# Kernel optimization log

Hardware: AMD Instinct MI355X
Metric: run time of the kernel (lower is better)

Reference implementation:

```python
import jax, jax.numpy as jnp
import numpy as np

N_HEADS = 16
ROPE_DIMS = 64


def _rope_tables(T, rd):
    # freqs: 1 / 10000^(arange(0, rd, 2)/rd), shape [rd//2]
    freqs = 1.0 / (10000.0 ** (np.arange(0, rd, 2, dtype=np.float32) / np.float32(rd)))
    ang = np.outer(np.arange(T, dtype=np.float32), freqs)  # [T, rd//2]
    return jnp.asarray(np.cos(ang)), jnp.asarray(np.sin(ang))


def _apply_rope(x, cos, sin, rd):
    # x: [B, H, T, D]; rotate-half style on first rd dims
    x_rope, x_pass = x[..., :rd], x[..., rd:]
    x1, x2 = x_rope[..., : rd // 2], x_rope[..., rd // 2 :]
    c = cos[None, None]  # [1,1,T,rd//2]
    s = sin[None, None]
    x_rot = jnp.concatenate([x1 * c - x2 * s, x2 * c + x1 * s], axis=-1)
    return jnp.concatenate([x_rot, x_pass], axis=-1)


def setup_inputs() -> dict:
    key = jax.random.key(0)
    k1, k2, k3 = jax.random.split(key, 3)
    B, T, C = 32, 512, 2048
    x = jax.random.normal(k1, (B, T, C), dtype=jnp.float32)
    w_qkv = jax.random.normal(k2, (3 * C, C), dtype=jnp.float32) * 0.02
    w_out = jax.random.normal(k3, (C, C), dtype=jnp.float32) * 0.02
    return {"x": x, "w_qkv": w_qkv, "w_out": w_out}


def reference(x, w_qkv, w_out):
    B, T, C = x.shape
    H = N_HEADS
    D = C // H
    # fused QKV projection: F.linear(x, w) = x @ w.T
    qkv = jnp.einsum('btc,fc->btf', x, w_qkv).reshape(B, T, 3, H, D)
    q = jnp.transpose(qkv[:, :, 0], (0, 2, 1, 3))  # [B,H,T,D]
    k = jnp.transpose(qkv[:, :, 1], (0, 2, 1, 3))
    v = jnp.transpose(qkv[:, :, 2], (0, 2, 1, 3))
    cos, sin = _rope_tables(T, ROPE_DIMS)
    q = _apply_rope(q, cos, sin, ROPE_DIMS)
    k = _apply_rope(k, cos, sin, ROPE_DIMS)
    # causal SDPA
    scale = 1.0 / jnp.sqrt(jnp.asarray(D, dtype=x.dtype))
    scores = jnp.einsum('bhqd,bhkd->bhqk', q, k) * scale
    causal = jnp.tril(jnp.ones((T, T), dtype=bool))
    scores = jnp.where(causal[None, None], scores, jnp.finfo(scores.dtype).min)
    attn = jax.nn.softmax(scores, axis=-1)
    y = jnp.einsum('bhqk,bhkd->bhqd', attn, v)
    y = jnp.transpose(y, (0, 2, 1, 3)).reshape(B, T, C)
    return jnp.einsum('btc,fc->btf', y, w_out)
```

## Files before the change

kernel.cpp:

```cpp
#include <hip/hip_runtime.h>


typedef __bf16 bf16x8 __attribute__((ext_vector_type(8)));
typedef float floatx4 __attribute__((ext_vector_type(4)));

__device__ __forceinline__ unsigned short f2bf(float f) {
  union { float f; unsigned u; } v; v.f = f;
  unsigned r = v.u + 0x7FFFu + ((v.u >> 16) & 1u);
  return (unsigned short)(r >> 16);
}
__device__ __forceinline__ float bf2f(unsigned short h) {
  union { unsigned u; float f; } v; v.u = ((unsigned)h) << 16; return v.f;
}

__device__ __forceinline__ void load_lds16(const void* g, void* l) {
  __builtin_amdgcn_global_load_lds((__attribute__((address_space(1))) void*)g,
                                   (__attribute__((address_space(3))) void*)l,
                                   16, 0, 0);
}

__global__ void rope_tables(float* __restrict__ cost, float* __restrict__ sint) {
  int i = blockIdx.x * 256 + threadIdx.x;
  if (i >= 512 * 32) return;
  int t = i >> 5, f = i & 31;
  float e = -(float)(2 * f) / 64.0f;
  float freq = powf(10000.0f, e);
  float ang = (float)t * freq;
  cost[i] = cosf(ang);
  sint[i] = sinf(ang);
}

__global__ void cast_bf16(const float* __restrict__ in,
                          unsigned short* __restrict__ out, int n8) {
  int i = blockIdx.x * 256 + threadIdx.x;
  if (i >= n8) return;
  float4 a = ((const float4*)in)[2 * i];
  float4 b = ((const float4*)in)[2 * i + 1];
  union { uint4 v; unsigned short u[8]; } o;
  o.u[0] = f2bf(a.x); o.u[1] = f2bf(a.y); o.u[2] = f2bf(a.z); o.u[3] = f2bf(a.w);
  o.u[4] = f2bf(b.x); o.u[5] = f2bf(b.y); o.u[6] = f2bf(b.z); o.u[7] = f2bf(b.w);
  ((uint4*)out)[i] = o.v;
}

template <int OUT_BF16>
__global__ __launch_bounds__(256) void gemm_bt(
    const unsigned short* __restrict__ A, const unsigned short* __restrict__ Bt,
    void* __restrict__ Cout, int M, int N, int K) {
  __shared__ __align__(16) unsigned short As[128 * 64];
  __shared__ __align__(16) unsigned short Bs[128 * 64];
  const int tid = threadIdx.x;
  const int bn = blockIdx.x, bm = blockIdx.y;
  const int w = tid >> 6, l = tid & 63;
  const int quad = l >> 4, cl = l & 15;
  const int m_base = (w & 1) * 64, n_base = (w >> 1) * 64;
  floatx4 acc[4][4] = {};

  const int srow = tid >> 3;
  const int sc = (tid & 7) ^ (srow & 7);
  const unsigned short* Ag = A + (size_t)(bm * 128 + srow) * K + sc * 8;
  const unsigned short* Bg = Bt + (size_t)(bn * 128 + srow) * K + sc * 8;
  unsigned short* asd = As + tid * 8;
  unsigned short* bsd = Bs + tid * 8;

  for (int kt = 0; kt < K; kt += 64) {
    __syncthreads();
#pragma unroll
    for (int i = 0; i < 4; ++i) {
      load_lds16(Ag + (size_t)i * 32 * K + kt, asd + i * 32 * 64);
      load_lds16(Bg + (size_t)i * 32 * K + kt, bsd + i * 32 * 64);
    }
    __syncthreads();
#pragma unroll
    for (int k0 = 0; k0 < 64; k0 += 32) {
      const int xs = (((k0 >> 3) + quad) ^ (cl & 7)) << 3;
      bf16x8 a[4], b[4];
#pragma unroll
      for (int mt = 0; mt < 4; ++mt)
        a[mt] = *(const bf16x8*)(As + (m_base + mt * 16 + cl) * 64 + xs);
#pragma unroll
      for (int nt = 0; nt < 4; ++nt)
        b[nt] = *(const bf16x8*)(Bs + (n_base + nt * 16 + cl) * 64 + xs);
#pragma unroll
      for (int mt = 0; mt < 4; ++mt)
#pragma unroll
        for (int nt = 0; nt < 4; ++nt)
          acc[mt][nt] = __builtin_amdgcn_mfma_f32_16x16x32_bf16(
              a[mt], b[nt], acc[mt][nt], 0, 0, 0);
    }
  }
#pragma unroll
  for (int mt = 0; mt < 4; ++mt)
#pragma unroll
    for (int nt = 0; nt < 4; ++nt)
#pragma unroll
      for (int r = 0; r < 4; ++r) {
        int gm = bm * 128 + m_base + mt * 16 + quad * 4 + r;
        int gn = bn * 128 + n_base + nt * 16 + cl;
        float v = acc[mt][nt][r];
        if (OUT_BF16)
          ((unsigned short*)Cout)[(size_t)gm * N + gn] = f2bf(v);
        else
          ((float*)Cout)[(size_t)gm * N + gn] = v;
      }
}

__global__ __launch_bounds__(256) void attn_kernel(
    const unsigned short* __restrict__ qkv, const float* __restrict__ cost,
    const float* __restrict__ sint, unsigned short* __restrict__ y) {
  __shared__ __align__(16) unsigned short Qs[64][136];
  __shared__ __align__(16) unsigned short Ks[64][136];
  __shared__ __align__(16) unsigned short VTs[128][64];
  __shared__ __align__(16) unsigned short Ps[4][16][72];

  const int bh = blockIdx.x, qt = blockIdx.y;
  const int b = bh >> 4, h = bh & 15;
  const int tid = threadIdx.x, w = tid >> 6, l = tid & 63;
  const int quad = l >> 4, cl = l & 15;
  const float scale = 0.08838834764831845f * 1.4426950408889634f;

  {
    const int r = tid >> 2, j = tid & 3;
    const int tg = qt * 64 + r;
    const unsigned short* qrow = qkv + (size_t)(b * 512 + tg) * 6144 + h * 128;
    union { uint4 v; unsigned short u[8]; } c1, c2, p1, p2, o1, o2, o3, o4;
    c1.v = *(const uint4*)(qrow + j * 8);
    c2.v = *(const uint4*)(qrow + j * 8 + 32);
    p1.v = *(const uint4*)(qrow + 64 + j * 16);
    p2.v = *(const uint4*)(qrow + 64 + j * 16 + 8);
#pragma unroll
    for (int jj = 0; jj < 8; ++jj) {
      int d = j * 8 + jj;
      float c = cost[tg * 32 + d], s = sint[tg * 32 + d];
      float x1 = bf2f(c1.u[jj]), x2 = bf2f(c2.u[jj]);
      o1.u[jj] = f2bf((x1 * c - x2 * s) * scale);
      o2.u[jj] = f2bf((x2 * c + x1 * s) * scale);
      o3.u[jj] = f2bf(bf2f(p1.u[jj]) * scale);
      o4.u[jj] = f2bf(bf2f(p2.u[jj]) * scale);
    }
    *(uint4*)&Qs[r][j * 8]          = o1.v;
    *(uint4*)&Qs[r][j * 8 + 32]     = o2.v;
    *(uint4*)&Qs[r][64 + j * 16]     = o3.v;
    *(uint4*)&Qs[r][64 + j * 16 + 8] = o4.v;
  }

  floatx4 o[8] = {};
  float m_i[4] = {-__builtin_inff(), -__builtin_inff(), -__builtin_inff(),
                  -__builtin_inff()};
  float l_i[4] = {0.f, 0.f, 0.f, 0.f};

  for (int ktile = 0; ktile <= qt; ++ktile) {
    __syncthreads();
    {
      const int r = tid >> 2, j = tid & 3;
      const int tg = ktile * 64 + r;
      const unsigned short* krow =
          qkv + (size_t)(b * 512 + tg) * 6144 + 2048 + h * 128;
      union { uint4 v; unsigned short u[8]; } c1, c2, p1, p2, o1, o2;
      c1.v = *(const uint4*)(krow + j * 8);
      c2.v = *(const uint4*)(krow + j * 8 + 32);
      p1.v = *(const uint4*)(krow + 64 + j * 16);
      p2.v = *(const uint4*)(krow + 64 + j * 16 + 8);
#pragma unroll
      for (int jj = 0; jj < 8; ++jj) {
        int d = j * 8 + jj;
        float c = cost[tg * 32 + d], s = sint[tg * 32 + d];
        float x1 = bf2f(c1.u[jj]), x2 = bf2f(c2.u[jj]);
        o1.u[jj] = f2bf(x1 * c - x2 * s);
        o2.u[jj] = f2bf(x2 * c + x1 * s);
      }
      *(uint4*)&Ks[r][j * 8]          = o1.v;
      *(uint4*)&Ks[r][j * 8 + 32]     = o2.v;
      *(uint4*)&Ks[r][64 + j * 16]     = p1.v;
      *(uint4*)&Ks[r][64 + j * 16 + 8] = p2.v;
    }
    {
      const int rowg = tid >> 5;
      const int colg = tid & 31;
      const int kk0 = rowg * 8, d0 = colg * 4;
      const unsigned short* vbase = qkv +
          (size_t)(b * 512 + ktile * 64 + kk0) * 6144 + 4096 + h * 128 + d0;
      uint2 rv[8];
#pragma unroll
      for (int rr = 0; rr < 8; ++rr)
        rv[rr] = *(const uint2*)(vbase + (size_t)rr * 6144);
#pragma unroll
      for (int c = 0; c < 4; ++c) {
        const int d = d0 + c;
        unsigned out[4];
#pragma unroll
        for (int p = 0; p < 4; ++p) {
          unsigned ua = ((const unsigned*)&rv[2 * p])[c >> 1];
          unsigned ub = ((const unsigned*)&rv[2 * p + 1])[c >> 1];
          unsigned lo = (c & 1) ? (ua >> 16) : (ua & 0xffffu);
          unsigned hi = (c & 1) ? (ub >> 16) : (ub & 0xffffu);
          out[p] = lo | (hi << 16);
        }
        *(uint4*)&VTs[d][(rowg ^ (d & 7)) << 3] = *(uint4*)out;
      }
    }
    __syncthreads();

    floatx4 s[4] = {};
#pragma unroll
    for (int kc = 0; kc < 4; ++kc) {
      bf16x8 aq = *(const bf16x8*)(&Qs[w * 16 + cl][kc * 32 + quad * 8]);
#pragma unroll
      for (int nt = 0; nt < 4; ++nt) {
        bf16x8 bk = *(const bf16x8*)(&Ks[nt * 16 + cl][kc * 32 + quad * 8]);
        s[nt] = __builtin_amdgcn_mfma_f32_16x16x32_bf16(aq, bk, s[nt], 0, 0, 0);
      }
    }
    if (ktile == qt) {
#pragma unroll
      for (int nt = 0; nt < 4; ++nt)
#pragma unroll
        for (int r = 0; r < 4; ++r) {
          int qrow_l = w * 16 + quad * 4 + r;
          int kcol_l = nt * 16 + cl;
          if (kcol_l > qrow_l) s[nt][r] = -__builtin_inff();
        }
    }
#pragma unroll
    for (int r = 0; r < 4; ++r) {
      float mx = fmaxf(fmaxf(s[0][r], s[1][r]), fmaxf(s[2][r], s[3][r]));
      mx = fmaxf(mx, __shfl_xor(mx, 1));
      mx = fmaxf(mx, __shfl_xor(mx, 2));
      mx = fmaxf(mx, __shfl_xor(mx, 4));
      mx = fmaxf(mx, __shfl_xor(mx, 8));
      float mn = fmaxf(m_i[r], mx);
      float a = exp2f(m_i[r] - mn);
      float rs = 0.f;
#pragma unroll
      for (int nt = 0; nt < 4; ++nt) {
        float p = exp2f(s[nt][r] - mn);
        s[nt][r] = p;
        rs += p;
      }
      rs += __shfl_xor(rs, 1);
      rs += __shfl_xor(rs, 2);
      rs += __shfl_xor(rs, 4);
      rs += __shfl_xor(rs, 8);
      l_i[r] = l_i[r] * a + rs;
      m_i[r] = mn;
#pragma unroll
      for (int nt2 = 0; nt2 < 8; ++nt2) o[nt2][r] *= a;
#pragma unroll
      for (int nt = 0; nt < 4; ++nt)
        Ps[w][quad * 4 + r][nt * 16 + cl] = f2bf(s[nt][r]);
    }
    __syncthreads();

#pragma unroll
    for (int kc2 = 0; kc2 < 2; ++kc2) {
      bf16x8 ap = *(const bf16x8*)(&Ps[w][cl][kc2 * 32 + quad * 8]);
#pragma unroll
      for (int nt2 = 0; nt2 < 8; ++nt2) {
        bf16x8 bv = *(const bf16x8*)(
            &VTs[nt2 * 16 + cl][((kc2 * 4 + quad) ^ (cl & 7)) << 3]);
        o[nt2] = __builtin_amdgcn_mfma_f32_16x16x32_bf16(ap, bv, o[nt2], 0, 0, 0);
      }
    }
  }

#pragma unroll
  for (int r = 0; r < 4; ++r) {
    float inv = 1.0f / l_i[r];
    size_t row =
        (size_t)(b * 512 + qt * 64 + w * 16 + quad * 4 + r) * 2048 + h * 128;
#pragma unroll
    for (int nt2 = 0; nt2 < 8; ++nt2)
      y[row + nt2 * 16 + cl] = f2bf(o[nt2][r] * inv);
  }
}

extern "C" void kernel_launch(void* const* d_in, const int* in_sizes, int n_in,
                              void* d_out, int out_size, void* d_ws,
                              size_t ws_size, hipStream_t stream) {
  const float* x = (const float*)d_in[0];
  const float* wqkv = (const float*)d_in[1];
  const float* wout = (const float*)d_in[2];
  float* out = (float*)d_out;

  char* ws = (char*)d_ws;
  float* cost = (float*)ws;            ws += (size_t)512 * 32 * 4;
  float* sint = (float*)ws;            ws += (size_t)512 * 32 * 4;
  unsigned short* xb = (unsigned short*)ws;    ws += (size_t)16384 * 2048 * 2;
  unsigned short* wqkvb = (unsigned short*)ws; ws += (size_t)6144 * 2048 * 2;
  unsigned short* woutb = (unsigned short*)ws; ws += (size_t)2048 * 2048 * 2;
  unsigned short* qkvb = (unsigned short*)ws;  ws += (size_t)16384 * 6144 * 2;
  unsigned short* yb = (unsigned short*)ws;    ws += (size_t)16384 * 2048 * 2;

  rope_tables<<<dim3(64), dim3(256), 0, stream>>>(cost, sint);
  cast_bf16<<<dim3(16384), dim3(256), 0, stream>>>(x, xb, 33554432 / 8);
  cast_bf16<<<dim3(6144), dim3(256), 0, stream>>>(wqkv, wqkvb, 12582912 / 8);
  cast_bf16<<<dim3(2048), dim3(256), 0, stream>>>(wout, woutb, 4194304 / 8);
  gemm_bt<1><<<dim3(48, 128), dim3(256), 0, stream>>>(xb, wqkvb, (void*)qkvb,
                                                      16384, 6144, 2048);
  attn_kernel<<<dim3(512, 8), dim3(256), 0, stream>>>(qkvb, cost, sint, yb);
  gemm_bt<0><<<dim3(16, 128), dim3(256), 0, stream>>>(yb, woutb, (void*)out,
                                                      16384, 2048, 2048);
}
```

Measured before the change: 1.039 ms.

## Replace GEMM with 256x256 double-buffered pipelined kernel and grid swizzle

```diff
diff --git a/kernel.cpp b/kernel.cpp
--- a/kernel.cpp
+++ b/kernel.cpp
@@ -18,6 +18,11 @@
                                    (__attribute__((address_space(3))) void*)l,
                                    16, 0, 0);
 }
+
+#define BARRIER() asm volatile("s_barrier" ::: "memory")
+#define VMCNT6()  asm volatile("s_waitcnt vmcnt(6)" ::: "memory")
+#define VMCNT0()  asm volatile("s_waitcnt vmcnt(0)" ::: "memory")
+#define LGKM0()   asm volatile("s_waitcnt lgkmcnt(0)" ::: "memory")
 
 __global__ void rope_tables(float* __restrict__ cost, float* __restrict__ sint) {
   int i = blockIdx.x * 256 + threadIdx.x;
@@ -43,60 +48,141 @@
 }
 
 template <int OUT_BF16>
-__global__ __launch_bounds__(256) void gemm_bt(
+__global__ __launch_bounds__(512, 2) void gemm256(
     const unsigned short* __restrict__ A, const unsigned short* __restrict__ Bt,
     void* __restrict__ Cout, int M, int N, int K) {
-  __shared__ __align__(16) unsigned short As[128 * 64];
-  __shared__ __align__(16) unsigned short Bs[128 * 64];
+  __shared__ __align__(16) unsigned short As[2][16384];
+  __shared__ __align__(16) unsigned short Bs[2][16384];
+
   const int tid = threadIdx.x;
-  const int bn = blockIdx.x, bm = blockIdx.y;
+  const int nbx = gridDim.x;
+  const int nwg = nbx * gridDim.y;
+  const int lin = blockIdx.y * nbx + blockIdx.x;
+  const int swz = (lin & 7) * (nwg >> 3) + (lin >> 3);
+  const int bm = swz / nbx, bn = swz % nbx;
+
   const int w = tid >> 6, l = tid & 63;
+  const int wm = w >> 2, wn = w & 3;
   const int quad = l >> 4, cl = l & 15;
-  const int m_base = (w & 1) * 64, n_base = (w >> 1) * 64;
-  floatx4 acc[4][4] = {};
+  const int xs0 = ((0 + quad) ^ (cl & 7)) << 3;
+  const int xs1 = ((4 + quad) ^ (cl & 7)) << 3;
+  const int aoff = (wm * 128 + cl) * 64;
+  const int boff = (wn * 64 + cl) * 64;
 
   const int srow = tid >> 3;
-  const int sc = (tid & 7) ^ (srow & 7);
-  const unsigned short* Ag = A + (size_t)(bm * 128 + srow) * K + sc * 8;
-  const unsigned short* Bg = Bt + (size_t)(bn * 128 + srow) * K + sc * 8;
-  unsigned short* asd = As + tid * 8;
-  unsigned short* bsd = Bs + tid * 8;
-
-  for (int kt = 0; kt < K; kt += 64) {
-    __syncthreads();
-#pragma unroll
-    for (int i = 0; i < 4; ++i) {
-      load_lds16(Ag + (size_t)i * 32 * K + kt, asd + i * 32 * 64);
-      load_lds16(Bg + (size_t)i * 32 * K + kt, bsd + i * 32 * 64);
-    }
-    __syncthreads();
-#pragma unroll
-    for (int k0 = 0; k0 < 64; k0 += 32) {
-      const int xs = (((k0 >> 3) + quad) ^ (cl & 7)) << 3;
-      bf16x8 a[4], b[4];
-#pragma unroll
-      for (int mt = 0; mt < 4; ++mt)
-        a[mt] = *(const bf16x8*)(As + (m_base + mt * 16 + cl) * 64 + xs);
-#pragma unroll
-      for (int nt = 0; nt < 4; ++nt)
-        b[nt] = *(const bf16x8*)(Bs + (n_base + nt * 16 + cl) * 64 + xs);
-#pragma unroll
-      for (int mt = 0; mt < 4; ++mt)
-#pragma unroll
-        for (int nt = 0; nt < 4; ++nt)
-          acc[mt][nt] = __builtin_amdgcn_mfma_f32_16x16x32_bf16(
-              a[mt], b[nt], acc[mt][nt], 0, 0, 0);
-    }
+  const int lc = (tid & 7) ^ (srow & 7);
+  const unsigned short* Ag = A + (size_t)(bm * 256 + srow) * K + lc * 8;
+  const unsigned short* Bg = Bt + (size_t)(bn * 256 + srow) * K + lc * 8;
+
+  auto stageA = [&](int q, int h, int k0) {
+    const unsigned short* src = Ag + (size_t)(h * 128) * K + k0;
+    unsigned short* dst = &As[q][0] + h * 8192 + tid * 8;
+    load_lds16(src, dst);
+    load_lds16(src + (size_t)64 * K, dst + 4096);
+  };
+  auto stageB = [&](int q, int h, int k0) {
+    const unsigned short* src = Bg + (size_t)(h * 128) * K + k0;
+    unsigned short* dst = &Bs[q][0] + h * 8192 + tid * 8;
+    load_lds16(src, dst);
+    load_lds16(src + (size_t)64 * K, dst + 4096);
+  };
+
+  floatx4 acc[8][4] = {};
+  const int NT = K >> 6;
+
+  stageA(0, 0, 0);  stageA(0, 1, 0);  stageB(0, 0, 0);  stageB(0, 1, 0);
+  stageA(1, 0, 64); stageA(1, 1, 64); stageB(1, 0, 64);
+  VMCNT6();
+  BARRIER();
+
+  for (int t = 0; t < NT; ++t) {
+    const int q = t & 1;
+    const unsigned short* pA = &As[q][0] + aoff;
+    const unsigned short* pB = &Bs[q][0] + boff;
+    const int k2 = (t + 2) << 6;
+    const bool s2 = (t + 2) < NT;
+
+    bf16x8 a[8][2], b[2][2];
+#pragma unroll
+    for (int mi = 0; mi < 8; ++mi) {
+      a[mi][0] = *(const bf16x8*)(pA + mi * 1024 + xs0);
+      a[mi][1] = *(const bf16x8*)(pA + mi * 1024 + xs1);
+    }
+#pragma unroll
+    for (int ni = 0; ni < 2; ++ni) {
+      b[ni][0] = *(const bf16x8*)(pB + ni * 1024 + xs0);
+      b[ni][1] = *(const bf16x8*)(pB + ni * 1024 + xs1);
+    }
+    if (t + 1 < NT) stageB(q ^ 1, 1, (t + 1) << 6);
+    BARRIER();
+    __builtin_amdgcn_s_setprio(1);
+#pragma unroll
+    for (int mi = 0; mi < 4; ++mi)
+#pragma unroll
+      for (int ni = 0; ni < 2; ++ni)
+#pragma unroll
+        for (int ks = 0; ks < 2; ++ks)
+          acc[mi][ni] = __builtin_amdgcn_mfma_f32_16x16x32_bf16(
+              a[mi][ks], b[ni][ks], acc[mi][ni], 0, 0, 0);
+    __builtin_amdgcn_s_setprio(0);
+    LGKM0();
+    BARRIER();
+    if (s2) stageA(q, 0, k2);
+    BARRIER();
+    __builtin_amdgcn_s_setprio(1);
+#pragma unroll
+    for (int mi = 4; mi < 8; ++mi)
+#pragma unroll
+      for (int ni = 0; ni < 2; ++ni)
+#pragma unroll
+        for (int ks = 0; ks < 2; ++ks)
+          acc[mi][ni] = __builtin_amdgcn_mfma_f32_16x16x32_bf16(
+              a[mi][ks], b[ni][ks], acc[mi][ni], 0, 0, 0);
+    __builtin_amdgcn_s_setprio(0);
+    BARRIER();
+#pragma unroll
+    for (int ni = 0; ni < 2; ++ni) {
+      b[ni][0] = *(const bf16x8*)(pB + (ni + 2) * 1024 + xs0);
+      b[ni][1] = *(const bf16x8*)(pB + (ni + 2) * 1024 + xs1);
+    }
+    if (s2) stageA(q, 1, k2);
+    BARRIER();
+    __builtin_amdgcn_s_setprio(1);
+#pragma unroll
+    for (int mi = 0; mi < 4; ++mi)
+#pragma unroll
+      for (int ni = 0; ni < 2; ++ni)
+#pragma unroll
+        for (int ks = 0; ks < 2; ++ks)
+          acc[mi][ni + 2] = __builtin_amdgcn_mfma_f32_16x16x32_bf16(
+              a[mi][ks], b[ni][ks], acc[mi][ni + 2], 0, 0, 0);
+    __builtin_amdgcn_s_setprio(0);
+    BARRIER();
+    if (s2) stageB(q, 0, k2);
+    BARRIER();
+    __builtin_amdgcn_s_setprio(1);
+#pragma unroll
+    for (int mi = 4; mi < 8; ++mi)
+#pragma unroll
+      for (int ni = 0; ni < 2; ++ni)
+#pragma unroll
+        for (int ks = 0; ks < 2; ++ks)
+          acc[mi][ni + 2] = __builtin_amdgcn_mfma_f32_16x16x32_bf16(
+              a[mi][ks], b[ni][ks], acc[mi][ni + 2], 0, 0, 0);
+    __builtin_amdgcn_s_setprio(0);
+    if (t < NT - 2) { VMCNT6(); } else { VMCNT0(); }
+    BARRIER();
   }
-#pragma unroll
-  for (int mt = 0; mt < 4; ++mt)
-#pragma unroll
-    for (int nt = 0; nt < 4; ++nt)
+
+#pragma unroll
+  for (int mi = 0; mi < 8; ++mi)
+#pragma unroll
+    for (int ni = 0; ni < 4; ++ni)
 #pragma unroll
       for (int r = 0; r < 4; ++r) {
-        int gm = bm * 128 + m_base + mt * 16 + quad * 4 + r;
-        int gn = bn * 128 + n_base + nt * 16 + cl;
-        float v = acc[mt][nt][r];
+        const int gm = bm * 256 + wm * 128 + mi * 16 + quad * 4 + r;
+        const int gn = bn * 256 + wn * 64 + ni * 16 + cl;
+        const float v = acc[mi][ni][r];
         if (OUT_BF16)
           ((unsigned short*)Cout)[(size_t)gm * N + gn] = f2bf(v);
         else
@@ -294,9 +380,9 @@
   cast_bf16<<<dim3(16384), dim3(256), 0, stream>>>(x, xb, 33554432 / 8);
   cast_bf16<<<dim3(6144), dim3(256), 0, stream>>>(wqkv, wqkvb, 12582912 / 8);
   cast_bf16<<<dim3(2048), dim3(256), 0, stream>>>(wout, woutb, 4194304 / 8);
-  gemm_bt<1><<<dim3(48, 128), dim3(256), 0, stream>>>(xb, wqkvb, (void*)qkvb,
-                                                      16384, 6144, 2048);
+  gemm256<1><<<dim3(24, 64), dim3(512), 0, stream>>>(xb, wqkvb, (void*)qkvb,
+                                                     16384, 6144, 2048);
   attn_kernel<<<dim3(512, 8), dim3(256), 0, stream>>>(qkvb, cost, sint, yb);
-  gemm_bt<0><<<dim3(16, 128), dim3(256), 0, stream>>>(yb, woutb, (void*)out,
-                                                      16384, 2048, 2048);
-}
+  gemm256<0><<<dim3(8, 64), dim3(512), 0, stream>>>(yb, woutb, (void*)out,
+                                                    16384, 2048, 2048);
+}
```

Measured after the change: 981.4 us. -5.6%, faster.
